# Kernel tuning notes

Hardware: AMD Instinct MI355X
Metric: run time of the kernel (lower is better)

Reference implementation:

```python
import jax, jax.numpy as jnp
import numpy as np

VOCAB, EMB_DIM = 50000, 300
HIDDEN, OUT_DIM, N_ASPECTS = 256, 3, 8
BATCH, SEQ = 8192, 128


def setup_inputs() -> dict:
    key = jax.random.key(0)
    k1, k2, k3, k4, k5, k6, k7 = jax.random.split(key, 7)
    input_ids = jax.random.randint(k1, (BATCH, SEQ), 0, VOCAB, dtype=jnp.int64 if jax.config.jax_enable_x64 else jnp.int32)
    aspect_id = jax.random.randint(k2, (BATCH,), 0, N_ASPECTS, dtype=jnp.int32)
    emb = jax.random.normal(k3, (VOCAB, EMB_DIM), dtype=jnp.float32)
    # Per-aspect 2-layer MLP params, stacked along aspect axis. PyTorch Linear
    # init scale ~ U(-1/sqrt(fan_in), 1/sqrt(fan_in)).
    s1 = 1.0 / np.sqrt(EMB_DIM)
    s2 = 1.0 / np.sqrt(HIDDEN)
    W1 = jax.random.uniform(k4, (N_ASPECTS, EMB_DIM, HIDDEN), jnp.float32, -s1, s1)
    b1 = jax.random.uniform(k5, (N_ASPECTS, HIDDEN), jnp.float32, -s1, s1)
    W2 = jax.random.uniform(k6, (N_ASPECTS, HIDDEN, OUT_DIM), jnp.float32, -s2, s2)
    b2 = jax.random.uniform(k7, (N_ASPECTS, OUT_DIM), jnp.float32, -s2, s2)
    return {"input_ids": input_ids, "aspect_id": aspect_id, "emb": emb,
            "W1": W1, "b1": b1, "W2": W2, "b2": b2}


def reference(input_ids, aspect_id, emb, W1, b1, W2, b2):
    # Embedding lookup + mean-pool over sequence -> [B, EMB_DIM]
    x = emb[input_ids].mean(axis=1)
    # Run every sample through every aspect MLP (A is tiny: 8), then select.
    # Same math as per-sample routed MLP, but as A batched GEMMs.
    h = jax.nn.relu(jnp.einsum('bd,adh->abh', x, W1) + b1[:, None, :])  # [A,B,H]
    o = jnp.einsum('abh,aho->abo', h, W2) + b2[:, None, :]              # [A,B,O]
    # Select per-sample expert output: [B, OUT_DIM]
    o_b = jnp.transpose(o, (1, 0, 2))  # [B, A, O]
    return jnp.take_along_axis(o_b, aspect_id[:, None, None], axis=1)[:, 0, :]
```

## Files before the change

### kernel.cpp

```cpp
#include <hip/hip_runtime.h>

constexpr int EMB_DIM   = 300;
constexpr int HIDDEN    = 256;
constexpr int OUT_DIM   = 3;
constexpr int SEQ       = 128;
constexpr int N_ASPECTS = 8;
constexpr int TILE      = 32;
constexpr int MTILE     = 8;

__device__ __forceinline__ unsigned int bfbits(float f) {
  unsigned int u = __float_as_uint(f);
  return (u + 0x7fffu + ((u >> 16) & 1u)) >> 16;
}
__device__ __forceinline__ unsigned int pack2(float lo, float hi) {
  return bfbits(lo) | (bfbits(hi) << 16);
}
__device__ __forceinline__ float blo(unsigned int u) { return __uint_as_float(u << 16); }
__device__ __forceinline__ float bhi(unsigned int u) { return __uint_as_float(u & 0xffff0000u); }

__global__ __launch_bounds__(1024) void prep_kernel(
    const float* __restrict__ emb, unsigned int* __restrict__ emb16, int n8,
    const float* __restrict__ W1, unsigned int* __restrict__ w16, int nw8,
    const int* __restrict__ aspect, int B, int* __restrict__ perm, int nperm) {
  const int t = threadIdx.x;

  if (blockIdx.x != 0) {
    int i = (blockIdx.x - 1) * 1024 + t;
    const int stride = (gridDim.x - 1) * 1024;
    const int total8 = n8 + nw8;
    for (; i < total8; i += stride) {
      const float4* p;
      unsigned int* dst;
      int k;
      if (i < n8) { p = (const float4*)emb + (size_t)i * 2;        dst = emb16; k = i; }
      else        { p = (const float4*)W1  + (size_t)(i - n8) * 2; dst = w16;   k = i - n8; }
      float4 a = p[0], b = p[1];
      uint4 o;
      o.x = pack2(a.x, a.y); o.y = pack2(a.z, a.w);
      o.z = pack2(b.x, b.y); o.w = pack2(b.z, b.w);
      ((uint4*)dst)[k] = o;
    }
    return;
  }

  const int lane = t & 63, wave = t >> 6;
  __shared__ int wcnt[16][N_ASPECTS];
  __shared__ int cur[16][N_ASPECTS];

  for (int i = t; i < nperm; i += 1024) perm[i] = -1;

  int my_a[8];
  int cnt[N_ASPECTS];
#pragma unroll
  for (int q = 0; q < N_ASPECTS; ++q) cnt[q] = 0;
#pragma unroll
  for (int k = 0; k < 8; ++k) {
    int s = t + k * 1024;
    int a = (s < B) ? aspect[s] : -1;
    my_a[k] = a;
#pragma unroll
    for (int q = 0; q < N_ASPECTS; ++q) cnt[q] += (a == q);
  }
#pragma unroll
  for (int q = 0; q < N_ASPECTS; ++q) {
    int c = cnt[q];
    for (int off = 32; off > 0; off >>= 1) c += __shfl_down(c, off);
    if (lane == 0) wcnt[wave][q] = c;
  }
  __syncthreads();
  if (t == 0) {
    int base = 0;
    for (int q = 0; q < N_ASPECTS; ++q) {
      int tot = 0;
      for (int w = 0; w < 16; ++w) { cur[w][q] = base + tot; tot += wcnt[w][q]; }
      base += ((tot + TILE - 1) / TILE) * TILE;
    }
  }
  __syncthreads();

#pragma unroll
  for (int k = 0; k < 8; ++k) {
    int a = my_a[k];
    int s = t + k * 1024;
#pragma unroll
    for (int q = 0; q < N_ASPECTS; ++q) {
      unsigned long long m = __ballot(a == q);
      if (a == q) {
        int rank = __popcll(m & ((1ull << lane) - 1ull));
        int pos = cur[wave][q] + rank;
        perm[pos] = s;
        if (rank == __popcll(m) - 1) cur[wave][q] = pos + 1;
      }
    }
  }
}

__global__ __launch_bounds__(256) void fused_kernel(
    const int* __restrict__ ids, const unsigned short* __restrict__ emb16,
    const int* __restrict__ aspect, const int* __restrict__ perm,
    const unsigned short* __restrict__ w16, const float* __restrict__ b1,
    const float* __restrict__ W2, const float* __restrict__ b2,
    float* __restrict__ out) {
  const int t = threadIdx.x;
  const int wave = t >> 6, lane = t & 63;
  const int start = blockIdx.x * MTILE;

  __shared__ int            ss[MTILE];
  __shared__ unsigned short sid[MTILE][SEQ];
  __shared__ float          xs[MTILE][EMB_DIM];
  __shared__ float          xch[2][4][64][4];

  if (t < MTILE) ss[t] = perm[start + t];
  __syncthreads();
  const int s0 = ss[0];
  if (s0 < 0) return;
  const int a = aspect[s0];

  const int sa = 2 * wave, sb = 2 * wave + 1;
  const int ma = __builtin_amdgcn_readfirstlane(ss[sa] < 0 ? s0 : ss[sa]);
  const int mb = __builtin_amdgcn_readfirstlane(ss[sb] < 0 ? s0 : ss[sb]);

  int r0 = ids[(size_t)ma * SEQ + lane];
  int r1 = ids[(size_t)ma * SEQ + lane + 64];
  int r2 = ids[(size_t)mb * SEQ + lane];
  int r3 = ids[(size_t)mb * SEQ + lane + 64];

#pragma unroll
  for (int k = 2; k <= 128; k <<= 1) {
#pragma unroll
    for (int j = k >> 1; j >= 1; j >>= 1) {
      if (j == 64) {
        int lo0 = min(r0, r1), hi0 = max(r0, r1);
        int lo1 = min(r2, r3), hi1 = max(r2, r3);
        r0 = lo0; r1 = hi0; r2 = lo1; r3 = hi1;
      } else {
        const bool up0 = ((lane & k) == 0);
        const bool up1 = (((lane + 64) & k) == 0);
        const bool side = ((lane & j) == 0);
        int o0 = __shfl_xor(r0, j);
        int o1 = __shfl_xor(r1, j);
        int o2 = __shfl_xor(r2, j);
        int o3 = __shfl_xor(r3, j);
        r0 = (side == up0) ? min(r0, o0) : max(r0, o0);
        r1 = (side == up1) ? min(r1, o1) : max(r1, o1);
        r2 = (side == up0) ? min(r2, o2) : max(r2, o2);
        r3 = (side == up1) ? min(r3, o3) : max(r3, o3);
      }
    }
  }

  sid[sa][lane]      = (unsigned short)r0;
  sid[sa][lane + 64] = (unsigned short)r1;
  sid[sb][lane]      = (unsigned short)r2;
  sid[sb][lane + 64] = (unsigned short)r3;

  float p0 = 0.f, p1 = 0.f, p2 = 0.f, p3 = 0.f;
  float q0 = 0.f, q1 = 0.f, q2 = 0.f, q3 = 0.f;
  float ta0 = 0.f, ta1 = 0.f, ta2 = 0.f, ta3 = 0.f;
  float tb0 = 0.f, tb1 = 0.f, tb2 = 0.f, tb3 = 0.f;
  const bool tail = (lane < 11);

#pragma unroll 4
  for (int s = 0; s < SEQ; ++s) {
    const uint2* __restrict__ ra =
        (const uint2*)(emb16 + (size_t)sid[sa][s] * EMB_DIM);
    const uint2* __restrict__ rb =
        (const uint2*)(emb16 + (size_t)sid[sb][s] * EMB_DIM);
    uint2 va = ra[lane];
    uint2 vb = rb[lane];
    p0 += blo(va.x); p1 += bhi(va.x); p2 += blo(va.y); p3 += bhi(va.y);
    q0 += blo(vb.x); q1 += bhi(vb.x); q2 += blo(vb.y); q3 += bhi(vb.y);
    if (tail) {
      uint2 wa = ra[64 + lane];
      uint2 wb = rb[64 + lane];
      ta0 += blo(wa.x); ta1 += bhi(wa.x); ta2 += blo(wa.y); ta3 += bhi(wa.y);
      tb0 += blo(wb.x); tb1 += bhi(wb.x); tb2 += blo(wb.y); tb3 += bhi(wb.y);
    }
  }

  const float sc = 1.0f / (float)SEQ;
  *(float4*)&xs[sa][4 * lane] = make_float4(p0 * sc, p1 * sc, p2 * sc, p3 * sc);
  *(float4*)&xs[sb][4 * lane] = make_float4(q0 * sc, q1 * sc, q2 * sc, q3 * sc);
  if (tail) {
    *(float4*)&xs[sa][256 + 4 * lane] =
        make_float4(ta0 * sc, ta1 * sc, ta2 * sc, ta3 * sc);
    *(float4*)&xs[sb][256 + 4 * lane] =
        make_float4(tb0 * sc, tb1 * sc, tb2 * sc, tb3 * sc);
  }
  __syncthreads();

  const int g = wave >> 1;
  const int kw = wave & 1;

  int smp[4];
#pragma unroll
  for (int s = 0; s < 4; ++s)
    smp[s] = __builtin_amdgcn_readfirstlane(ss[g * 4 + s]);

  const unsigned short* __restrict__ w1r =
      w16 + (size_t)a * EMB_DIM * HIDDEN + 4 * lane;
  float4 acc[4];
  if (kw == 0) {
    const float4 bb = ((const float4*)(b1 + a * HIDDEN))[lane];
#pragma unroll
    for (int s = 0; s < 4; ++s) acc[s] = bb;
  } else {
#pragma unroll
    for (int s = 0; s < 4; ++s) acc[s] = make_float4(0.f, 0.f, 0.f, 0.f);
  }
  const int d0 = kw ? 160 : 0;
  const int d1 = kw ? EMB_DIM : 160;
#pragma unroll 2
  for (int d = d0; d < d1; d += 4) {
    float4 xv[4];
#pragma unroll
    for (int s = 0; s < 4; ++s) xv[s] = *(const float4*)&xs[g * 4 + s][d];
#pragma unroll
    for (int dd = 0; dd < 4; ++dd) {
      const uint2 wv = *(const uint2*)(w1r + (size_t)(d + dd) * HIDDEN);
      const float w0 = blo(wv.x), w1v = bhi(wv.x);
      const float w2v = blo(wv.y), w3v = bhi(wv.y);
#pragma unroll
      for (int s = 0; s < 4; ++s) {
        const float xsc = dd == 0 ? xv[s].x : dd == 1 ? xv[s].y
                         : dd == 2 ? xv[s].z : xv[s].w;
        acc[s].x = fmaf(xsc, w0,  acc[s].x);
        acc[s].y = fmaf(xsc, w1v, acc[s].y);
        acc[s].z = fmaf(xsc, w2v, acc[s].z);
        acc[s].w = fmaf(xsc, w3v, acc[s].w);
      }
    }
  }

  if (kw == 0) {
    *(float4*)&xch[g][2][lane][0] = acc[2];
    *(float4*)&xch[g][3][lane][0] = acc[3];
  } else {
    *(float4*)&xch[g][0][lane][0] = acc[0];
    *(float4*)&xch[g][1][lane][0] = acc[1];
  }
  __syncthreads();

  const float4* __restrict__ w2p =
      (const float4*)(W2 + (size_t)a * HIDDEN * OUT_DIM + lane * 12);
  const float4 w2a = w2p[0];
  const float4 w2b = w2p[1];
  const float4 w2c = w2p[2];

  float4 own[2];
  int ms[2];
  if (kw == 0) {
    own[0] = acc[0]; own[1] = acc[1];
    ms[0] = smp[0];  ms[1] = smp[1];
  } else {
    own[0] = acc[2]; own[1] = acc[3];
    ms[0] = smp[2];  ms[1] = smp[3];
  }
  const int mys = 2 * kw;

  float pp[2][OUT_DIM];
#pragma unroll
  for (int i = 0; i < 2; ++i) {
    const float4 pr = *(const float4*)&xch[g][mys + i][lane][0];
    const float h0 = fmaxf(own[i].x + pr.x, 0.f);
    const float h1 = fmaxf(own[i].y + pr.y, 0.f);
    const float h2 = fmaxf(own[i].z + pr.z, 0.f);
    const float h3 = fmaxf(own[i].w + pr.w, 0.f);
    pp[i][0] = fmaf(h0, w2a.x, fmaf(h1, w2a.w, fmaf(h2, w2b.z, h3 * w2c.y)));
    pp[i][1] = fmaf(h0, w2a.y, fmaf(h1, w2b.x, fmaf(h2, w2b.w, h3 * w2c.z)));
    pp[i][2] = fmaf(h0, w2a.z, fmaf(h1, w2b.y, fmaf(h2, w2c.x, h3 * w2c.w)));
  }
#pragma unroll
  for (int off = 32; off > 0; off >>= 1)
#pragma unroll
    for (int i = 0; i < 2; ++i) {
      pp[i][0] += __shfl_down(pp[i][0], off);
      pp[i][1] += __shfl_down(pp[i][1], off);
      pp[i][2] += __shfl_down(pp[i][2], off);
    }

  if (lane == 0) {
    const float g0 = b2[a * OUT_DIM + 0];
    const float g1 = b2[a * OUT_DIM + 1];
    const float g2 = b2[a * OUT_DIM + 2];
#pragma unroll
    for (int i = 0; i < 2; ++i) {
      if (ms[i] >= 0) {
        float* o = out + (size_t)ms[i] * OUT_DIM;
        o[0] = pp[i][0] + g0;
        o[1] = pp[i][1] + g1;
        o[2] = pp[i][2] + g2;
      }
    }
  }
}

extern "C" void kernel_launch(void* const* d_in, const int* in_sizes, int n_in,
                              void* d_out, int out_size, void* d_ws, size_t ws_size,
                              hipStream_t stream) {
  const int*   ids    = (const int*)d_in[0];
  const int*   aspect = (const int*)d_in[1];
  const float* emb    = (const float*)d_in[2];
  const float* W1     = (const float*)d_in[3];
  const float* b1     = (const float*)d_in[4];
  const float* W2     = (const float*)d_in[5];
  const float* b2     = (const float*)d_in[6];
  float*       out    = (float*)d_out;

  const int B     = in_sizes[1];
  const int nemb  = in_sizes[2];
  const int nw1   = in_sizes[3];
  const int nblk  = (B + TILE - 1) / TILE + N_ASPECTS;
  const int nperm = nblk * TILE;

  int* perm = (int*)d_ws;
  unsigned short* emb16 =
      (unsigned short*)((char*)perm + (((size_t)nperm * 4 + 15) & ~(size_t)15));
  unsigned short* w16 = emb16 + (size_t)nemb;

  prep_kernel<<<513, 1024, 0, stream>>>(emb, (unsigned int*)emb16, nemb / 8,
                                        W1, (unsigned int*)w16, nw1 / 8,
                                        aspect, B, perm, nperm);
  fused_kernel<<<nperm / MTILE, 256, 0, stream>>>(ids, emb16, aspect, perm,
                                                  w16, b1, W2, b2, out);
}
```

Baseline: 120.6 us.

## Shrink fused tile to 4 samples with per-wave full-K MLP, drop LDS exchange

Each block now handles 4 samples with 2 waves. Each wave computes the full 300-deep first-layer GEMV for its own two samples, so the K-split across waves, the shared-memory partial-sum exchange and two block barriers go away. The cost is that each W1 row slice is reused across only 2 samples instead of 4. That doubles W1 reads from cache per sample, and twice as many blocks are launched.

```diff
diff --git a/kernel.cpp b/kernel.cpp
--- a/kernel.cpp
+++ b/kernel.cpp
@@ -6,7 +6,7 @@
 constexpr int SEQ       = 128;
 constexpr int N_ASPECTS = 8;
 constexpr int TILE      = 32;
-constexpr int MTILE     = 8;
+constexpr int MTILE     = 4;
 
 __device__ __forceinline__ unsigned int bfbits(float f) {
   unsigned int u = __float_as_uint(f);
@@ -95,7 +95,7 @@
   }
 }
 
-__global__ __launch_bounds__(256) void fused_kernel(
+__global__ __launch_bounds__(128) void fused_kernel(
     const int* __restrict__ ids, const unsigned short* __restrict__ emb16,
     const int* __restrict__ aspect, const int* __restrict__ perm,
     const unsigned short* __restrict__ w16, const float* __restrict__ b1,
@@ -108,7 +108,6 @@
   __shared__ int            ss[MTILE];
   __shared__ unsigned short sid[MTILE][SEQ];
   __shared__ float          xs[MTILE][EMB_DIM];
-  __shared__ float          xch[2][4][64][4];
 
   if (t < MTILE) ss[t] = perm[start + t];
   __syncthreads();
@@ -117,8 +116,10 @@
   const int a = aspect[s0];
 
   const int sa = 2 * wave, sb = 2 * wave + 1;
-  const int ma = __builtin_amdgcn_readfirstlane(ss[sa] < 0 ? s0 : ss[sa]);
-  const int mb = __builtin_amdgcn_readfirstlane(ss[sb] < 0 ? s0 : ss[sb]);
+  const int msA = __builtin_amdgcn_readfirstlane(ss[sa]);
+  const int msB = __builtin_amdgcn_readfirstlane(ss[sb]);
+  const int ma = msA < 0 ? s0 : msA;
+  const int mb = msB < 0 ? s0 : msB;
 
   int r0 = ids[(size_t)ma * SEQ + lane];
   int r1 = ids[(size_t)ma * SEQ + lane + 64];
@@ -187,59 +188,33 @@
     *(float4*)&xs[sb][256 + 4 * lane] =
         make_float4(tb0 * sc, tb1 * sc, tb2 * sc, tb3 * sc);
   }
-  __syncthreads();
-
-  const int g = wave >> 1;
-  const int kw = wave & 1;
-
-  int smp[4];
-#pragma unroll
-  for (int s = 0; s < 4; ++s)
-    smp[s] = __builtin_amdgcn_readfirstlane(ss[g * 4 + s]);
 
   const unsigned short* __restrict__ w1r =
       w16 + (size_t)a * EMB_DIM * HIDDEN + 4 * lane;
-  float4 acc[4];
-  if (kw == 0) {
-    const float4 bb = ((const float4*)(b1 + a * HIDDEN))[lane];
-#pragma unroll
-    for (int s = 0; s < 4; ++s) acc[s] = bb;
-  } else {
-#pragma unroll
-    for (int s = 0; s < 4; ++s) acc[s] = make_float4(0.f, 0.f, 0.f, 0.f);
-  }
-  const int d0 = kw ? 160 : 0;
-  const int d1 = kw ? EMB_DIM : 160;
+  const float4 bb = ((const float4*)(b1 + a * HIDDEN))[lane];
+  float4 acc0 = bb, acc1 = bb;
+
 #pragma unroll 2
-  for (int d = d0; d < d1; d += 4) {
-    float4 xv[4];
-#pragma unroll
-    for (int s = 0; s < 4; ++s) xv[s] = *(const float4*)&xs[g * 4 + s][d];
+  for (int d = 0; d < EMB_DIM; d += 4) {
+    float4 xv0 = *(const float4*)&xs[sa][d];
+    float4 xv1 = *(const float4*)&xs[sb][d];
 #pragma unroll
     for (int dd = 0; dd < 4; ++dd) {
       const uint2 wv = *(const uint2*)(w1r + (size_t)(d + dd) * HIDDEN);
       const float w0 = blo(wv.x), w1v = bhi(wv.x);
       const float w2v = blo(wv.y), w3v = bhi(wv.y);
-#pragma unroll
-      for (int s = 0; s < 4; ++s) {
-        const float xsc = dd == 0 ? xv[s].x : dd == 1 ? xv[s].y
-                         : dd == 2 ? xv[s].z : xv[s].w;
-        acc[s].x = fmaf(xsc, w0,  acc[s].x);
-        acc[s].y = fmaf(xsc, w1v, acc[s].y);
-        acc[s].z = fmaf(xsc, w2v, acc[s].z);
-        acc[s].w = fmaf(xsc, w3v, acc[s].w);
-      }
-    }
-  }
-
-  if (kw == 0) {
-    *(float4*)&xch[g][2][lane][0] = acc[2];
-    *(float4*)&xch[g][3][lane][0] = acc[3];
-  } else {
-    *(float4*)&xch[g][0][lane][0] = acc[0];
-    *(float4*)&xch[g][1][lane][0] = acc[1];
-  }
-  __syncthreads();
+      const float x0 = dd == 0 ? xv0.x : dd == 1 ? xv0.y : dd == 2 ? xv0.z : xv0.w;
+      const float x1 = dd == 0 ? xv1.x : dd == 1 ? xv1.y : dd == 2 ? xv1.z : xv1.w;
+      acc0.x = fmaf(x0, w0,  acc0.x);
+      acc0.y = fmaf(x0, w1v, acc0.y);
+      acc0.z = fmaf(x0, w2v, acc0.z);
+      acc0.w = fmaf(x0, w3v, acc0.w);
+      acc1.x = fmaf(x1, w0,  acc1.x);
+      acc1.y = fmaf(x1, w1v, acc1.y);
+      acc1.z = fmaf(x1, w2v, acc1.z);
+      acc1.w = fmaf(x1, w3v, acc1.w);
+    }
+  }
 
   const float4* __restrict__ w2p =
       (const float4*)(W2 + (size_t)a * HIDDEN * OUT_DIM + lane * 12);
@@ -247,50 +222,39 @@
   const float4 w2b = w2p[1];
   const float4 w2c = w2p[2];
 
-  float4 own[2];
-  int ms[2];
-  if (kw == 0) {
-    own[0] = acc[0]; own[1] = acc[1];
-    ms[0] = smp[0];  ms[1] = smp[1];
-  } else {
-    own[0] = acc[2]; own[1] = acc[3];
-    ms[0] = smp[2];  ms[1] = smp[3];
-  }
-  const int mys = 2 * kw;
-
-  float pp[2][OUT_DIM];
-#pragma unroll
-  for (int i = 0; i < 2; ++i) {
-    const float4 pr = *(const float4*)&xch[g][mys + i][lane][0];
-    const float h0 = fmaxf(own[i].x + pr.x, 0.f);
-    const float h1 = fmaxf(own[i].y + pr.y, 0.f);
-    const float h2 = fmaxf(own[i].z + pr.z, 0.f);
-    const float h3 = fmaxf(own[i].w + pr.w, 0.f);
-    pp[i][0] = fmaf(h0, w2a.x, fmaf(h1, w2a.w, fmaf(h2, w2b.z, h3 * w2c.y)));
-    pp[i][1] = fmaf(h0, w2a.y, fmaf(h1, w2b.x, fmaf(h2, w2b.w, h3 * w2c.z)));
-    pp[i][2] = fmaf(h0, w2a.z, fmaf(h1, w2b.y, fmaf(h2, w2c.x, h3 * w2c.w)));
-  }
-#pragma unroll
-  for (int off = 32; off > 0; off >>= 1)
-#pragma unroll
-    for (int i = 0; i < 2; ++i) {
-      pp[i][0] += __shfl_down(pp[i][0], off);
-      pp[i][1] += __shfl_down(pp[i][1], off);
-      pp[i][2] += __shfl_down(pp[i][2], off);
-    }
+  const float ha0 = fmaxf(acc0.x, 0.f), ha1 = fmaxf(acc0.y, 0.f);
+  const float ha2 = fmaxf(acc0.z, 0.f), ha3 = fmaxf(acc0.w, 0.f);
+  const float hb0 = fmaxf(acc1.x, 0.f), hb1 = fmaxf(acc1.y, 0.f);
+  const float hb2 = fmaxf(acc1.z, 0.f), hb3 = fmaxf(acc1.w, 0.f);
+
+  float pa0 = fmaf(ha0, w2a.x, fmaf(ha1, w2a.w, fmaf(ha2, w2b.z, ha3 * w2c.y)));
+  float pa1 = fmaf(ha0, w2a.y, fmaf(ha1, w2b.x, fmaf(ha2, w2b.w, ha3 * w2c.z)));
+  float pa2 = fmaf(ha0, w2a.z, fmaf(ha1, w2b.y, fmaf(ha2, w2c.x, ha3 * w2c.w)));
+  float pb0 = fmaf(hb0, w2a.x, fmaf(hb1, w2a.w, fmaf(hb2, w2b.z, hb3 * w2c.y)));
+  float pb1 = fmaf(hb0, w2a.y, fmaf(hb1, w2b.x, fmaf(hb2, w2b.w, hb3 * w2c.z)));
+  float pb2 = fmaf(hb0, w2a.z, fmaf(hb1, w2b.y, fmaf(hb2, w2c.x, hb3 * w2c.w)));
+
+#pragma unroll
+  for (int off = 32; off > 0; off >>= 1) {
+    pa0 += __shfl_down(pa0, off);
+    pa1 += __shfl_down(pa1, off);
+    pa2 += __shfl_down(pa2, off);
+    pb0 += __shfl_down(pb0, off);
+    pb1 += __shfl_down(pb1, off);
+    pb2 += __shfl_down(pb2, off);
+  }
 
   if (lane == 0) {
     const float g0 = b2[a * OUT_DIM + 0];
     const float g1 = b2[a * OUT_DIM + 1];
     const float g2 = b2[a * OUT_DIM + 2];
-#pragma unroll
-    for (int i = 0; i < 2; ++i) {
-      if (ms[i] >= 0) {
-        float* o = out + (size_t)ms[i] * OUT_DIM;
-        o[0] = pp[i][0] + g0;
-        o[1] = pp[i][1] + g1;
-        o[2] = pp[i][2] + g2;
-      }
+    if (msA >= 0) {
+      float* o = out + (size_t)msA * OUT_DIM;
+      o[0] = pa0 + g0; o[1] = pa1 + g1; o[2] = pa2 + g2;
+    }
+    if (msB >= 0) {
+      float* o = out + (size_t)msB * OUT_DIM;
+      o[0] = pb0 + g0; o[1] = pb1 + g1; o[2] = pb2 + g2;
     }
   }
 }
@@ -321,6 +285,6 @@
   prep_kernel<<<513, 1024, 0, stream>>>(emb, (unsigned int*)emb16, nemb / 8,
                                         W1, (unsigned int*)w16, nw1 / 8,
                                         aspect, B, perm, nperm);
-  fused_kernel<<<nperm / MTILE, 256, 0, stream>>>(ids, emb16, aspect, perm,
+  fused_kernel<<<nperm / MTILE, 128, 0, stream>>>(ids, emb16, aspect, perm,
                                                   w16, b1, W2, b2, out);
 }
```

After: 128.2 us. 1.06x slower.
